# Performance work log

Measured on AMD Instinct MI355X. Metric: run time of the kernel, lower is better.

## Reference

```python
import jax, jax.numpy as jnp
import numpy as np


def setup_inputs() -> dict:
    key = jax.random.key(0)
    k1, k2 = jax.random.split(key)
    N, C, H, W = 32, 1, 768, 1024
    inp = jax.random.normal(k1, (N, C, H, W), dtype=jnp.float32)
    # target values in {0,1,2}: 0=neg, 1=pos, 2=ignore
    tgt = jax.random.randint(k2, (N, C, H, W), 0, 3).astype(jnp.float32)
    return {"input": inp, "target": tgt}


def reference(input, target):
    # Flatten (NCHW -> NHWC -> flat); order is irrelevant for a mean reduction,
    # but we mirror the original transpose/view for faithfulness.
    x = jnp.transpose(input, (0, 2, 3, 1)).reshape(-1)
    t = jnp.transpose(target, (0, 2, 3, 1)).reshape(-1)

    pos = t == 1.0
    neg = t == 0.0
    pos_num = jnp.sum(pos).astype(x.dtype)
    neg_num = jnp.sum(neg).astype(x.dtype)
    sum_num = pos_num + neg_num

    # weight: neg_num/sum for positives, pos_num/sum for negatives, 0 for ignore (t>1)
    w = jnp.where(pos, neg_num / sum_num, jnp.where(neg, pos_num / sum_num, 0.0))

    # stable BCE-with-logits: max(x,0) - x*t + log1p(exp(-|x|))
    bce = jnp.maximum(x, 0.0) - x * t + jnp.log1p(jnp.exp(-jnp.abs(x)))
    return jnp.mean(w * bce)
```

## Files before the change

kernel.cpp:

```cpp
#include <hip/hip_runtime.h>


#define GRID1 2048
#define BLOCK 256

typedef float floatx4 __attribute__((ext_vector_type(4)));

__device__ __forceinline__ void do_elem(float xv, float tv,
                                        float& cp, float& cn,
                                        float& sp, float& sn) {
  float a = fabsf(xv);
  float e = __expf(-a);
  float l = __logf(1.0f + e);
  float c = fmaxf(xv, 0.f) + l;
  bool pos = (tv == 1.0f);
  bool neg = (tv == 0.0f);
  cp += pos ? 1.0f : 0.0f;
  cn += neg ? 1.0f : 0.0f;
  sp += pos ? (c - xv) : 0.0f;
  sn += neg ? c : 0.0f;
}

__device__ __forceinline__ void do_vec4(floatx4 xv, floatx4 tv,
                                        float& cp, float& cn,
                                        float& sp, float& sn) {
  do_elem(xv.x, tv.x, cp, cn, sp, sn);
  do_elem(xv.y, tv.y, cp, cn, sp, sn);
  do_elem(xv.z, tv.z, cp, cn, sp, sn);
  do_elem(xv.w, tv.w, cp, cn, sp, sn);
}

__global__ __launch_bounds__(BLOCK, 8) void edge_loss_stage1(
    const float* __restrict__ x, const float* __restrict__ t,
    float* __restrict__ partials, long long n) {
  long long n4 = n >> 2;
  long long per = (n4 + gridDim.x - 1) / gridDim.x;
  long long beg = (long long)blockIdx.x * per;
  long long end = beg + per < n4 ? beg + per : n4;

  const floatx4* __restrict__ x4 = (const floatx4*)x;
  const floatx4* __restrict__ t4 = (const floatx4*)t;

  float cp = 0.f, cn = 0.f, sp = 0.f, sn = 0.f;

  #pragma unroll 1
  for (long long i = beg + threadIdx.x; i < end; i += BLOCK) {
    floatx4 xv = __builtin_nontemporal_load(&x4[i]);
    floatx4 tv = __builtin_nontemporal_load(&t4[i]);
    do_vec4(xv, tv, cp, cn, sp, sn);
  }
  for (long long j = (n4 << 2) + (long long)blockIdx.x * BLOCK + threadIdx.x;
       j < n; j += (long long)gridDim.x * BLOCK) {
    do_elem(x[j], t[j], cp, cn, sp, sn);
  }

  #pragma unroll
  for (int off = 32; off > 0; off >>= 1) {
    cp += __shfl_down(cp, off, 64);
    cn += __shfl_down(cn, off, 64);
    sp += __shfl_down(sp, off, 64);
    sn += __shfl_down(sn, off, 64);
  }

  __shared__ float s_cp[4], s_cn[4], s_sp[4], s_sn[4];
  int lane = threadIdx.x & 63;
  int wave = threadIdx.x >> 6;
  if (lane == 0) { s_cp[wave] = cp; s_cn[wave] = cn; s_sp[wave] = sp; s_sn[wave] = sn; }
  __syncthreads();
  if (threadIdx.x == 0) {
    float tcp = 0.f, tcn = 0.f, tsp = 0.f, tsn = 0.f;
    #pragma unroll
    for (int k = 0; k < 4; ++k) { tcp += s_cp[k]; tcn += s_cn[k]; tsp += s_sp[k]; tsn += s_sn[k]; }
    int G = gridDim.x;
    partials[0 * G + blockIdx.x] = tcp;
    partials[1 * G + blockIdx.x] = tcn;
    partials[2 * G + blockIdx.x] = tsp;
    partials[3 * G + blockIdx.x] = tsn;
  }
}

__global__ __launch_bounds__(BLOCK) void edge_loss_stage2(
    const float* __restrict__ partials, float* __restrict__ out,
    int G, double inv_n) {
  double acc[4] = {0.0, 0.0, 0.0, 0.0};
  for (int i = threadIdx.x; i < G; i += BLOCK) {
    #pragma unroll
    for (int c = 0; c < 4; ++c) acc[c] += (double)partials[c * G + i];
  }
  #pragma unroll
  for (int off = 32; off > 0; off >>= 1) {
    #pragma unroll
    for (int c = 0; c < 4; ++c) acc[c] += __shfl_down(acc[c], off, 64);
  }
  __shared__ double s_acc[4][4];
  int lane = threadIdx.x & 63;
  int wave = threadIdx.x >> 6;
  if (lane == 0) {
    #pragma unroll
    for (int c = 0; c < 4; ++c) s_acc[wave][c] = acc[c];
  }
  __syncthreads();
  if (threadIdx.x == 0) {
    double pos = 0, neg = 0, spos = 0, sneg = 0;
    #pragma unroll
    for (int w = 0; w < 4; ++w) {
      pos += s_acc[w][0]; neg += s_acc[w][1];
      spos += s_acc[w][2]; sneg += s_acc[w][3];
    }
    double s = pos + neg;
    out[0] = (float)((neg * spos + pos * sneg) / s * inv_n);
  }
}

extern "C" void kernel_launch(void* const* d_in, const int* in_sizes, int n_in,
                              void* d_out, int out_size, void* d_ws, size_t ws_size,
                              hipStream_t stream) {
  const float* x = (const float*)d_in[0];
  const float* t = (const float*)d_in[1];
  long long n = (long long)in_sizes[0];
  float* partials = (float*)d_ws;

  edge_loss_stage1<<<GRID1, BLOCK, 0, stream>>>(x, t, partials, n);
  edge_loss_stage2<<<1, BLOCK, 0, stream>>>(partials, (float*)d_out,
                                            GRID1, 1.0 / (double)n);
}
```

Measured before the change: 197.9 us.

## Double-buffer input loads through LDS with async global_load_lds DMA

Replaces direct nontemporal vector loads in the stage-1 reduction with asynchronous global-to-LDS loads into a per-wave double buffer. The load for the next iteration is issued before the current one is computed, and waitcnt manages the vmcnt. The aim is to keep more memory requests in flight and hide load latency in this bandwidth-bound reduction. It adds 16 KB of LDS per block, which may limit occupancy, and it relies on hand-coded waitcnt encodings and the per-wave LDS layout that the 16-byte global_load_lds requires.

```diff
diff --git a/kernel.cpp b/kernel.cpp
--- a/kernel.cpp
+++ b/kernel.cpp
@@ -5,6 +5,15 @@
 #define BLOCK 256
 
 typedef float floatx4 __attribute__((ext_vector_type(4)));
+
+#define WAITCNT_VM2 0x0F72
+#define WAITCNT_VM0 0x0F70
+
+__device__ __forceinline__ void dma16nt(const floatx4* g, floatx4* l) {
+  __builtin_amdgcn_global_load_lds(
+      (const __attribute__((address_space(1))) void*)g,
+      (__attribute__((address_space(3))) void*)l, 16, 0,  2);
+}
 
 __device__ __forceinline__ void do_elem(float xv, float tv,
                                         float& cp, float& cn,
@@ -33,20 +42,53 @@
 __global__ __launch_bounds__(BLOCK, 8) void edge_loss_stage1(
     const float* __restrict__ x, const float* __restrict__ t,
     float* __restrict__ partials, long long n) {
+  __shared__ floatx4 lds[2][2][BLOCK];
+
   long long n4 = n >> 2;
   long long per = (n4 + gridDim.x - 1) / gridDim.x;
   long long beg = (long long)blockIdx.x * per;
   long long end = beg + per < n4 ? beg + per : n4;
+  long long len = end > beg ? end - beg : 0;
+  long long niter = len / BLOCK;
+
+  int lane = threadIdx.x & 63;
+  int wave = threadIdx.x >> 6;
 
   const floatx4* __restrict__ x4 = (const floatx4*)x;
   const floatx4* __restrict__ t4 = (const floatx4*)t;
 
   float cp = 0.f, cn = 0.f, sp = 0.f, sn = 0.f;
 
+  floatx4* lx0 = &lds[0][0][wave * 64];
+  floatx4* lt0 = &lds[0][1][wave * 64];
+  floatx4* lx1 = &lds[1][0][wave * 64];
+  floatx4* lt1 = &lds[1][1][wave * 64];
+
+  long long g = beg + threadIdx.x;
+  if (niter > 0) {
+    dma16nt(x4 + g, lx0);
+    dma16nt(t4 + g, lt0);
+  }
   #pragma unroll 1
-  for (long long i = beg + threadIdx.x; i < end; i += BLOCK) {
-    floatx4 xv = __builtin_nontemporal_load(&x4[i]);
-    floatx4 tv = __builtin_nontemporal_load(&t4[i]);
+  for (long long k = 0; k < niter; ++k) {
+    int cur = (int)(k & 1);
+    if (k + 1 < niter) {
+      long long gn = g + BLOCK;
+      dma16nt(x4 + gn, cur ? lx0 : lx1);
+      dma16nt(t4 + gn, cur ? lt0 : lt1);
+      __builtin_amdgcn_s_waitcnt(WAITCNT_VM2);
+    } else {
+      __builtin_amdgcn_s_waitcnt(WAITCNT_VM0);
+    }
+    __asm__ volatile("" ::: "memory");
+    floatx4 xv = (cur ? lx1 : lx0)[lane];
+    floatx4 tv = (cur ? lt1 : lt0)[lane];
+    do_vec4(xv, tv, cp, cn, sp, sn);
+    g += BLOCK;
+  }
+  if (g < end) {
+    floatx4 xv = __builtin_nontemporal_load(&x4[g]);
+    floatx4 tv = __builtin_nontemporal_load(&t4[g]);
     do_vec4(xv, tv, cp, cn, sp, sn);
   }
   for (long long j = (n4 << 2) + (long long)blockIdx.x * BLOCK + threadIdx.x;
@@ -63,8 +105,6 @@
   }
 
   __shared__ float s_cp[4], s_cn[4], s_sp[4], s_sn[4];
-  int lane = threadIdx.x & 63;
-  int wave = threadIdx.x >> 6;
   if (lane == 0) { s_cp[wave] = cp; s_cn[wave] = cn; s_sp[wave] = sp; s_sn[wave] = sn; }
   __syncthreads();
   if (threadIdx.x == 0) {
```

Result: no change. 199.8 us (+1.0%).
